# Kernel tuning notes

Measured on AMD Instinct MI355X. Metric: run time of the kernel, lower is better.

The kernel has to match this reference:

```python
import jax, jax.numpy as jnp
import numpy as np

B, T, C, H = 2, 2048, 1024, 16
D = C // H  # head dim = 64
EPS = 1e-5


def layernorm(x, g, b):
    mu = jnp.mean(x, axis=-1, keepdims=True)
    var = jnp.var(x, axis=-1, keepdims=True)
    return (x - mu) * jax.lax.rsqrt(var + EPS) * g + b


def setup_inputs() -> dict:
    key = jax.random.key(0)
    ks = jax.random.split(key, 8)
    init_scale = 0.25
    return {
        "x": jax.random.normal(ks[0], (B, T, C), dtype=jnp.float32),
        # weights stored [in, out] (transpose of torch Linear)
        "w_qkv": jax.random.normal(ks[1], (C, 3 * C), dtype=jnp.float32) * init_scale,
        "b_qkv": jnp.zeros((3 * C,), dtype=jnp.float32),
        "w_proj": jax.random.normal(ks[2], (C, C), dtype=jnp.float32) * init_scale,
        "b_proj": jnp.zeros((C,), dtype=jnp.float32),
        "ln1_g": jnp.ones((C,), dtype=jnp.float32),
        "ln1_b": jnp.zeros((C,), dtype=jnp.float32),
        "w_fc": jax.random.normal(ks[3], (C, 4 * C), dtype=jnp.float32) * init_scale,
        "b_fc": jnp.zeros((4 * C,), dtype=jnp.float32),
        "w_out": jax.random.normal(ks[4], (4 * C, C), dtype=jnp.float32) * init_scale,
        "b_out": jnp.zeros((C,), dtype=jnp.float32),
        "ln2_g": jnp.ones((C,), dtype=jnp.float32),
        "ln2_b": jnp.zeros((C,), dtype=jnp.float32),
    }


def reference(x, w_qkv, b_qkv, w_proj, b_proj, ln1_g, ln1_b,
              w_fc, b_fc, w_out, b_out, ln2_g, ln2_b):
    # ---- attention sub-block (pre-LN) ----
    h = layernorm(x, ln1_g, ln1_b)
    qkv = h @ w_qkv + b_qkv                      # [B,T,3C]
    q, k, v = jnp.split(qkv, 3, axis=-1)
    q = q.reshape(B, T, H, D)
    k = k.reshape(B, T, H, D)
    v = v.reshape(B, T, H, D)
    scores = jnp.einsum('bthd,bshd->bhts', q, k) * (1.0 / np.sqrt(D))
    attn = jax.nn.softmax(scores, axis=-1)       # full [B,H,T,T] as in source
    out = jnp.einsum('bhts,bshd->bthd', attn, v).reshape(B, T, C)
    x = x + out @ w_proj + b_proj
    # ---- MLP sub-block (pre-LN) ----
    h = layernorm(x, ln2_g, ln2_b)
    h = jax.nn.gelu(h @ w_fc + b_fc, approximate=False)  # torch nn.GELU default = exact
    x = x + h @ w_out + b_out
    return x
```

## Files before the change

### kernel.cpp

```cpp
#include <hip/hip_runtime.h>
#include <hip/hip_bf16.h>
#include <math.h>

#define DEVINL static __device__ __forceinline__

typedef _Float16 f16x8 __attribute__((ext_vector_type(8)));
typedef _Float16 f16x4 __attribute__((ext_vector_type(4)));
typedef float f32x4 __attribute__((ext_vector_type(4)));

constexpr int TT = 2048, CC = 1024, HH = 16, DD = 64;

DEVINL void gload_lds16(const void* g, void* s) {
  __builtin_amdgcn_global_load_lds(
      (const __attribute__((address_space(1))) void*)g,
      (__attribute__((address_space(3))) void*)s, 16, 0, 0);
}

__global__ __launch_bounds__(256) void transpose_cast(
    const float* __restrict__ in, _Float16* __restrict__ out, int K, int N) {
  __shared__ float tile[32][33];
  int n0 = blockIdx.x * 32, k0 = blockIdx.y * 32;
  int tx = threadIdx.x & 31, ty = threadIdx.x >> 5;
  #pragma unroll
  for (int i = 0; i < 32; i += 8)
    tile[ty + i][tx] = in[(size_t)(k0 + ty + i) * N + n0 + tx];
  __syncthreads();
  #pragma unroll
  for (int i = 0; i < 32; i += 8)
    out[(size_t)(n0 + ty + i) * K + k0 + tx] = (_Float16)tile[tx][ty + i];
}

__global__ __launch_bounds__(256) void ln_cast(
    const float* __restrict__ x, const float* __restrict__ g,
    const float* __restrict__ bta, _Float16* __restrict__ out) {
  int row = blockIdx.x, t = threadIdx.x;
  float4 v = ((const float4*)(x + (size_t)row * CC))[t];
  float s = v.x + v.y + v.z + v.w;
  float s2 = v.x * v.x + v.y * v.y + v.z * v.z + v.w * v.w;
  #pragma unroll
  for (int o = 32; o >= 1; o >>= 1) { s += __shfl_xor(s, o); s2 += __shfl_xor(s2, o); }
  __shared__ float ss[4], ssq[4];
  int w = t >> 6;
  if ((t & 63) == 0) { ss[w] = s; ssq[w] = s2; }
  __syncthreads();
  s = ss[0] + ss[1] + ss[2] + ss[3];
  s2 = ssq[0] + ssq[1] + ssq[2] + ssq[3];
  float mu = s * (1.0f / CC);
  float rs = rsqrtf(s2 * (1.0f / CC) - mu * mu + 1e-5f);
  float4 gv = ((const float4*)g)[t];
  float4 bv = ((const float4*)bta)[t];
  f16x4 o4;
  o4[0] = (_Float16)((v.x - mu) * rs * gv.x + bv.x);
  o4[1] = (_Float16)((v.y - mu) * rs * gv.y + bv.y);
  o4[2] = (_Float16)((v.z - mu) * rs * gv.z + bv.z);
  o4[3] = (_Float16)((v.w - mu) * rs * gv.w + bv.w);
  ((f16x4*)(out + (size_t)row * CC))[t] = o4;
}

template <int EPI, int N, int K>
__global__ __launch_bounds__(256) void gemm_bt(
    const _Float16* __restrict__ A, const _Float16* __restrict__ Bt,
    const float* __restrict__ bias, const float* __restrict__ res,
    void* __restrict__ outp) {
  __shared__ __align__(16) _Float16 As[128 * 64];
  __shared__ __align__(16) _Float16 Bs[128 * 64];
  const int bm0 = blockIdx.y * 128, bn0 = blockIdx.x * 128;
  const int t = threadIdx.x, w = t >> 6, l = t & 63, lg = l >> 4, lr = l & 15;
  const int wr = w >> 1, wc = w & 1;
  const int srow = t >> 3, sc = t & 7;
  f32x4 acc[4][4] = {};
  for (int k0 = 0; k0 < K; k0 += 64) {
    #pragma unroll
    for (int q = 0; q < 4; ++q) {
      int row = q * 32 + srow;
      int gc = sc ^ (row & 7);
      gload_lds16(A + (size_t)(bm0 + row) * K + k0 + gc * 8, As + row * 64 + sc * 8);
      gload_lds16(Bt + (size_t)(bn0 + row) * K + k0 + gc * 8, Bs + row * 64 + sc * 8);
    }
    __syncthreads();
    #pragma unroll
    for (int ks = 0; ks < 2; ++ks) {
      f16x8 af[4], bfr[4];
      #pragma unroll
      for (int mi = 0; mi < 4; ++mi) {
        int row = wr * 64 + mi * 16 + lr;
        af[mi] = *(const f16x8*)(As + row * 64 + (((ks * 4 + lg) ^ (row & 7)) << 3));
      }
      #pragma unroll
      for (int ni = 0; ni < 4; ++ni) {
        int row = wc * 64 + ni * 16 + lr;
        bfr[ni] = *(const f16x8*)(Bs + row * 64 + (((ks * 4 + lg) ^ (row & 7)) << 3));
      }
      #pragma unroll
      for (int mi = 0; mi < 4; ++mi)
        #pragma unroll
        for (int ni = 0; ni < 4; ++ni)
          acc[mi][ni] = __builtin_amdgcn_mfma_f32_16x16x32_f16(af[mi], bfr[ni], acc[mi][ni], 0, 0, 0);
    }
    __syncthreads();
  }
  #pragma unroll
  for (int mi = 0; mi < 4; ++mi) {
    #pragma unroll
    for (int ni = 0; ni < 4; ++ni) {
      int gc = bn0 + wc * 64 + ni * 16 + lr;
      float bv = bias[gc];
      #pragma unroll
      for (int r = 0; r < 4; ++r) {
        int gr = bm0 + wr * 64 + mi * 16 + lg * 4 + r;
        float v = acc[mi][ni][r] + bv;
        if constexpr (EPI == 1) {
          float gl = 0.5f * v * (1.0f + erff(v * 0.70710678118654752f));
          ((_Float16*)outp)[(size_t)gr * N + gc] = (_Float16)gl;
        } else {
          ((float*)outp)[(size_t)gr * N + gc] = res[(size_t)gr * N + gc] + v;
        }
      }
    }
  }
}

__global__ __launch_bounds__(256) void gemm_qkv(
    const _Float16* __restrict__ A, const _Float16* __restrict__ Bt,
    const float* __restrict__ bias,
    _Float16* __restrict__ qo, _Float16* __restrict__ ko,
    _Float16* __restrict__ vt) {
  __shared__ __align__(16) _Float16 As[128 * 64];
  __shared__ __align__(16) _Float16 Bs[128 * 64];
  const int bm0 = blockIdx.y * 128, bn0 = blockIdx.x * 128;
  const int t = threadIdx.x, w = t >> 6, l = t & 63, lg = l >> 4, lr = l & 15;
  const int wr = w >> 1, wc = w & 1;
  const int srow = t >> 3, sc = t & 7;
  f32x4 acc[4][4] = {};
  for (int k0 = 0; k0 < 1024; k0 += 64) {
    #pragma unroll
    for (int q = 0; q < 4; ++q) {
      int row = q * 32 + srow;
      int gc = sc ^ (row & 7);
      gload_lds16(A + (size_t)(bm0 + row) * 1024 + k0 + gc * 8, As + row * 64 + sc * 8);
      gload_lds16(Bt + (size_t)(bn0 + row) * 1024 + k0 + gc * 8, Bs + row * 64 + sc * 8);
    }
    __syncthreads();
    #pragma unroll
    for (int ks = 0; ks < 2; ++ks) {
      f16x8 af[4], bfr[4];
      #pragma unroll
      for (int mi = 0; mi < 4; ++mi) {
        int row = wr * 64 + mi * 16 + lr;
        af[mi] = *(const f16x8*)(As + row * 64 + (((ks * 4 + lg) ^ (row & 7)) << 3));
      }
      #pragma unroll
      for (int ni = 0; ni < 4; ++ni) {
        int row = wc * 64 + ni * 16 + lr;
        bfr[ni] = *(const f16x8*)(Bs + row * 64 + (((ks * 4 + lg) ^ (row & 7)) << 3));
      }
      #pragma unroll
      for (int mi = 0; mi < 4; ++mi)
        #pragma unroll
        for (int ni = 0; ni < 4; ++ni)
          acc[mi][ni] = __builtin_amdgcn_mfma_f32_16x16x32_f16(af[mi], bfr[ni], acc[mi][ni], 0, 0, 0);
    }
    __syncthreads();
  }
  const float QSCL = 0.125f * 1.44269504f;
  #pragma unroll
  for (int mi = 0; mi < 4; ++mi) {
    #pragma unroll
    for (int ni = 0; ni < 4; ++ni) {
      int gc = bn0 + wc * 64 + ni * 16 + lr;
      float bv = bias[gc];
      int sec = gc >> 10, cc = gc & 1023;
      #pragma unroll
      for (int r = 0; r < 4; ++r) {
        int gr = bm0 + wr * 64 + mi * 16 + lg * 4 + r;
        float v = acc[mi][ni][r] + bv;
        if (sec == 0) {
          qo[(size_t)gr * 1024 + cc] = (_Float16)(v * QSCL);
        } else if (sec == 1) {
          ko[(size_t)gr * 1024 + cc] = (_Float16)v;
        } else {
          int hh = cc >> 6, dd = cc & 63;
          int bb = gr >> 11, tk = gr & (TT - 1);
          vt[(((size_t)bb * HH + hh) * DD + dd) * TT + tk] = (_Float16)v;
        }
      }
    }
  }
}

__global__ __launch_bounds__(256) void flash_attn(
    const _Float16* __restrict__ qg, const _Float16* __restrict__ kg,
    const _Float16* __restrict__ vt, _Float16* __restrict__ att) {
  const int qt0 = blockIdx.x * 64, h = blockIdx.y, b = blockIdx.z;
  const int t = threadIdx.x, w = t >> 6, l = t & 63, lg = l >> 4, lr = l & 15;
  __shared__ __align__(16) _Float16 Ks[2][64 * 64];
  __shared__ __align__(16) _Float16 VTs[2][64 * 64];
  __shared__ __align__(16) _Float16 Ps[4][16 * 64];
  const int srow = t >> 3, sc = t & 7;
  f16x8 qf[2];
  #pragma unroll
  for (int ks = 0; ks < 2; ++ks)
    qf[ks] = *(const f16x8*)(qg + ((size_t)(b * TT + qt0 + w * 16 + lr)) * CC +
                             h * DD + ks * 32 + lg * 8);
  f32x4 o[4] = {};
  f32x4 osum = {};
  float mrow[4];
  #pragma unroll
  for (int r = 0; r < 4; ++r) mrow[r] = -3.0e38f;
  const f16x8 ones = {(_Float16)1, (_Float16)1, (_Float16)1, (_Float16)1,
                      (_Float16)1, (_Float16)1, (_Float16)1, (_Float16)1};

  auto STAGE = [&](int bufi, int kv0) {
    #pragma unroll
    for (int q = 0; q < 2; ++q) {
      int row = q * 32 + srow;
      int gc = sc ^ (row & 7);
      gload_lds16(kg + ((size_t)(b * TT + kv0 + row)) * CC + h * DD + gc * 8,
                  Ks[bufi] + row * 64 + sc * 8);
      gload_lds16(vt + (((size_t)b * HH + h) * DD + row) * TT + kv0 + gc * 8,
                  VTs[bufi] + row * 64 + sc * 8);
    }
  };
  STAGE(0, 0);
  __syncthreads();
  int cur = 0;
  for (int kv0 = 0; kv0 < TT; kv0 += 64) {
    if (kv0 + 64 < TT) STAGE(cur ^ 1, kv0 + 64);
    const _Float16* Kc = Ks[cur];
    const _Float16* Vc = VTs[cur];
    f32x4 s[4] = {};
    #pragma unroll
    for (int ks = 0; ks < 2; ++ks)
      #pragma unroll
      for (int ni = 0; ni < 4; ++ni) {
        int row = ni * 16 + lr;
        f16x8 kf = *(const f16x8*)(Kc + row * 64 + (((ks * 4 + lg) ^ (row & 7)) << 3));
        s[ni] = __builtin_amdgcn_mfma_f32_16x16x32_f16(qf[ks], kf, s[ni], 0, 0, 0);
      }
    float m4[4];
    int ok = 1;
    #pragma unroll
    for (int r = 0; r < 4; ++r) {
      m4[r] = fmaxf(fmaxf(s[0][r], s[1][r]), fmaxf(s[2][r], s[3][r]));
      ok &= (m4[r] <= mrow[r] + 8.0f) ? 1 : 0;
    }
    if (!__all(ok)) {
      #pragma unroll
      for (int r = 0; r < 4; ++r) {
        float rm = m4[r];
        #pragma unroll
        for (int msk = 1; msk <= 8; msk <<= 1) rm = fmaxf(rm, __shfl_xor(rm, msk));
        float mn = fmaxf(mrow[r], rm);
        float corr = exp2f(mrow[r] - mn);
        mrow[r] = mn;
        #pragma unroll
        for (int di = 0; di < 4; ++di) o[di][r] *= corr;
        osum[r] *= corr;
      }
    }
    _Float16* Pw = Ps[w];
    #pragma unroll
    for (int r = 0; r < 4; ++r) {
      float p0 = exp2f(s[0][r] - mrow[r]);
      float p1 = exp2f(s[1][r] - mrow[r]);
      float p2 = exp2f(s[2][r] - mrow[r]);
      float p3 = exp2f(s[3][r] - mrow[r]);
      int prow = lg * 4 + r, rx = prow & 7;
      Pw[prow * 64 + (((0 + (lr >> 3)) ^ rx) << 3) + (lr & 7)] = (_Float16)p0;
      Pw[prow * 64 + (((2 + (lr >> 3)) ^ rx) << 3) + (lr & 7)] = (_Float16)p1;
      Pw[prow * 64 + (((4 + (lr >> 3)) ^ rx) << 3) + (lr & 7)] = (_Float16)p2;
      Pw[prow * 64 + (((6 + (lr >> 3)) ^ rx) << 3) + (lr & 7)] = (_Float16)p3;
    }
    #pragma unroll
    for (int ks = 0; ks < 2; ++ks) {
      f16x8 pf = *(const f16x8*)(Pw + lr * 64 + (((ks * 4 + lg) ^ (lr & 7)) << 3));
      #pragma unroll
      for (int di = 0; di < 4; ++di) {
        int row = di * 16 + lr;
        f16x8 vf = *(const f16x8*)(Vc + row * 64 + (((ks * 4 + lg) ^ (row & 7)) << 3));
        o[di] = __builtin_amdgcn_mfma_f32_16x16x32_f16(pf, vf, o[di], 0, 0, 0);
      }
      osum = __builtin_amdgcn_mfma_f32_16x16x32_f16(pf, ones, osum, 0, 0, 0);
    }
    __syncthreads();
    cur ^= 1;
  }
  #pragma unroll
  for (int r = 0; r < 4; ++r) {
    float rinv = 1.0f / osum[r];
    int row_g = qt0 + w * 16 + lg * 4 + r;
    #pragma unroll
    for (int di = 0; di < 4; ++di)
      att[((size_t)(b * TT + row_g)) * CC + h * DD + di * 16 + lr] =
          (_Float16)(o[di][r] * rinv);
  }
}

extern "C" void kernel_launch(void* const* d_in, const int* in_sizes, int n_in,
                              void* d_out, int out_size, void* d_ws, size_t ws_size,
                              hipStream_t stream) {
  const float* x      = (const float*)d_in[0];
  const float* w_qkv  = (const float*)d_in[1];
  const float* b_qkv  = (const float*)d_in[2];
  const float* w_proj = (const float*)d_in[3];
  const float* b_proj = (const float*)d_in[4];
  const float* ln1_g  = (const float*)d_in[5];
  const float* ln1_b  = (const float*)d_in[6];
  const float* w_fc   = (const float*)d_in[7];
  const float* b_fc   = (const float*)d_in[8];
  const float* w_out  = (const float*)d_in[9];
  const float* b_out  = (const float*)d_in[10];
  const float* ln2_g  = (const float*)d_in[11];
  const float* ln2_b  = (const float*)d_in[12];

  char* ws = (char*)d_ws;
  _Float16* wqkv_t = (_Float16*)(ws);
  _Float16* wproj_t= (_Float16*)(ws + 6291456);
  _Float16* wfc_t  = (_Float16*)(ws + 8388608);
  _Float16* wout_t = (_Float16*)(ws + 16777216);
  _Float16* hslot  = (_Float16*)(ws + 25165824);
  _Float16* qbuf   = (_Float16*)(ws + 33554432);
  _Float16* kbuf   = (_Float16*)(ws + 41943040);
  _Float16* vtbuf  = (_Float16*)(ws + 50331648);
  _Float16* tbuf   = (_Float16*)(ws + 33554432);
  float*    x1     = (float*)(ws + 67108864);

  transpose_cast<<<dim3(96, 32), 256, 0, stream>>>(w_qkv, wqkv_t, 1024, 3072);
  transpose_cast<<<dim3(32, 32), 256, 0, stream>>>(w_proj, wproj_t, 1024, 1024);
  transpose_cast<<<dim3(128, 32), 256, 0, stream>>>(w_fc, wfc_t, 1024, 4096);
  transpose_cast<<<dim3(32, 128), 256, 0, stream>>>(w_out, wout_t, 4096, 1024);

  ln_cast<<<4096, 256, 0, stream>>>(x, ln1_g, ln1_b, hslot);
  gemm_qkv<<<dim3(24, 32), 256, 0, stream>>>(hslot, wqkv_t, b_qkv, qbuf, kbuf, vtbuf);
  flash_attn<<<dim3(32, 16, 2), 256, 0, stream>>>(qbuf, kbuf, vtbuf, hslot);
  gemm_bt<2, 1024, 1024><<<dim3(8, 32), 256, 0, stream>>>(hslot, wproj_t, b_proj, x, x1);
  ln_cast<<<4096, 256, 0, stream>>>(x1, ln2_g, ln2_b, hslot);
  gemm_bt<1, 4096, 1024><<<dim3(32, 32), 256, 0, stream>>>(hslot, wfc_t, b_fc, nullptr, tbuf);
  gemm_bt<2, 1024, 4096><<<dim3(8, 32), 256, 0, stream>>>(tbuf, wout_t, b_out, x1, (float*)d_out);
}
```

Measured before the change: 343.4 us.

## Narrow N-tiles for 1024-wide GEMMs and tune flash attention scheduling

The GEMM kernel gains a BN template parameter. The proj and out GEMMs (N=1024) now use 128x64 tiles, doubling their grid from 256 to 512 blocks so the CUs are better filled. Flash attention precomputes its swizzled LDS offsets and base pointers outside the loop, adds s_setprio around its MFMA sections, and sets a launch-bounds occupancy hint of 4. Narrower tiles lower per-block arithmetic intensity, and the occupancy hint may force register spills.

```diff
diff --git a/kernel.cpp b/kernel.cpp
--- a/kernel.cpp
+++ b/kernel.cpp
@@ -57,33 +57,40 @@
   ((f16x4*)(out + (size_t)row * CC))[t] = o4;
 }
 
-template <int EPI, int N, int K>
+template <int EPI, int N, int K, int BN>
 __global__ __launch_bounds__(256) void gemm_bt(
     const _Float16* __restrict__ A, const _Float16* __restrict__ Bt,
     const float* __restrict__ bias, const float* __restrict__ res,
     void* __restrict__ outp) {
+  constexpr int NWN = BN / 64;
+  constexpr int MI = 2 * NWN;
   __shared__ __align__(16) _Float16 As[128 * 64];
-  __shared__ __align__(16) _Float16 Bs[128 * 64];
-  const int bm0 = blockIdx.y * 128, bn0 = blockIdx.x * 128;
+  __shared__ __align__(16) _Float16 Bs[BN * 64];
+  const int bm0 = blockIdx.y * 128, bn0 = blockIdx.x * BN;
   const int t = threadIdx.x, w = t >> 6, l = t & 63, lg = l >> 4, lr = l & 15;
-  const int wr = w >> 1, wc = w & 1;
+  const int wr = w / NWN, wc = w % NWN;
   const int srow = t >> 3, sc = t & 7;
-  f32x4 acc[4][4] = {};
+  f32x4 acc[MI][4] = {};
   for (int k0 = 0; k0 < K; k0 += 64) {
     #pragma unroll
     for (int q = 0; q < 4; ++q) {
       int row = q * 32 + srow;
       int gc = sc ^ (row & 7);
       gload_lds16(A + (size_t)(bm0 + row) * K + k0 + gc * 8, As + row * 64 + sc * 8);
+    }
+    #pragma unroll
+    for (int q = 0; q < BN / 32; ++q) {
+      int row = q * 32 + srow;
+      int gc = sc ^ (row & 7);
       gload_lds16(Bt + (size_t)(bn0 + row) * K + k0 + gc * 8, Bs + row * 64 + sc * 8);
     }
     __syncthreads();
     #pragma unroll
     for (int ks = 0; ks < 2; ++ks) {
-      f16x8 af[4], bfr[4];
-      #pragma unroll
-      for (int mi = 0; mi < 4; ++mi) {
-        int row = wr * 64 + mi * 16 + lr;
+      f16x8 af[MI], bfr[4];
+      #pragma unroll
+      for (int mi = 0; mi < MI; ++mi) {
+        int row = wr * (16 * MI) + mi * 16 + lr;
         af[mi] = *(const f16x8*)(As + row * 64 + (((ks * 4 + lg) ^ (row & 7)) << 3));
       }
       #pragma unroll
@@ -92,7 +99,7 @@
         bfr[ni] = *(const f16x8*)(Bs + row * 64 + (((ks * 4 + lg) ^ (row & 7)) << 3));
       }
       #pragma unroll
-      for (int mi = 0; mi < 4; ++mi)
+      for (int mi = 0; mi < MI; ++mi)
         #pragma unroll
         for (int ni = 0; ni < 4; ++ni)
           acc[mi][ni] = __builtin_amdgcn_mfma_f32_16x16x32_f16(af[mi], bfr[ni], acc[mi][ni], 0, 0, 0);
@@ -100,14 +107,14 @@
     __syncthreads();
   }
   #pragma unroll
-  for (int mi = 0; mi < 4; ++mi) {
+  for (int mi = 0; mi < MI; ++mi) {
     #pragma unroll
     for (int ni = 0; ni < 4; ++ni) {
       int gc = bn0 + wc * 64 + ni * 16 + lr;
       float bv = bias[gc];
       #pragma unroll
       for (int r = 0; r < 4; ++r) {
-        int gr = bm0 + wr * 64 + mi * 16 + lg * 4 + r;
+        int gr = bm0 + wr * (16 * MI) + mi * 16 + lg * 4 + r;
         float v = acc[mi][ni][r] + bv;
         if constexpr (EPI == 1) {
           float gl = 0.5f * v * (1.0f + erff(v * 0.70710678118654752f));
@@ -188,7 +195,7 @@
   }
 }
 
-__global__ __launch_bounds__(256) void flash_attn(
+__global__ __launch_bounds__(256, 4) void flash_attn(
     const _Float16* __restrict__ qg, const _Float16* __restrict__ kg,
     const _Float16* __restrict__ vt, _Float16* __restrict__ att) {
   const int qt0 = blockIdx.x * 64, h = blockIdx.y, b = blockIdx.z;
@@ -197,6 +204,27 @@
   __shared__ __align__(16) _Float16 VTs[2][64 * 64];
   __shared__ __align__(16) _Float16 Ps[4][16 * 64];
   const int srow = t >> 3, sc = t & 7;
+  const int gcs = sc ^ (srow & 7);
+  const int dk0 = srow * 64 + sc * 8;
+  const _Float16* kg_b = kg + ((size_t)b * TT + srow) * CC + h * DD + gcs * 8;
+  const _Float16* vt_b = vt + (((size_t)b * HH + h) * DD + srow) * TT + gcs * 8;
+  int fro[2][4], pfo[2], pwo[4][4];
+  #pragma unroll
+  for (int ks = 0; ks < 2; ++ks) {
+    #pragma unroll
+    for (int ni = 0; ni < 4; ++ni) {
+      int row = ni * 16 + lr;
+      fro[ks][ni] = row * 64 + (((ks * 4 + lg) ^ (row & 7)) << 3);
+    }
+    pfo[ks] = lr * 64 + (((ks * 4 + lg) ^ (lr & 7)) << 3);
+  }
+  #pragma unroll
+  for (int r = 0; r < 4; ++r) {
+    int prow = lg * 4 + r, rx = prow & 7;
+    #pragma unroll
+    for (int ni = 0; ni < 4; ++ni)
+      pwo[r][ni] = prow * 64 + (((2 * ni + (lr >> 3)) ^ rx) << 3) + (lr & 7);
+  }
   f16x8 qf[2];
   #pragma unroll
   for (int ks = 0; ks < 2; ++ks)
@@ -213,12 +241,8 @@
   auto STAGE = [&](int bufi, int kv0) {
     #pragma unroll
     for (int q = 0; q < 2; ++q) {
-      int row = q * 32 + srow;
-      int gc = sc ^ (row & 7);
-      gload_lds16(kg + ((size_t)(b * TT + kv0 + row)) * CC + h * DD + gc * 8,
-                  Ks[bufi] + row * 64 + sc * 8);
-      gload_lds16(vt + (((size_t)b * HH + h) * DD + row) * TT + kv0 + gc * 8,
-                  VTs[bufi] + row * 64 + sc * 8);
+      gload_lds16(kg_b + (size_t)(kv0 + q * 32) * CC, Ks[bufi] + q * 2048 + dk0);
+      gload_lds16(vt_b + q * 32 * TT + kv0, VTs[bufi] + q * 2048 + dk0);
     }
   };
   STAGE(0, 0);
@@ -229,14 +253,15 @@
     const _Float16* Kc = Ks[cur];
     const _Float16* Vc = VTs[cur];
     f32x4 s[4] = {};
+    __builtin_amdgcn_s_setprio(1);
     #pragma unroll
     for (int ks = 0; ks < 2; ++ks)
       #pragma unroll
       for (int ni = 0; ni < 4; ++ni) {
-        int row = ni * 16 + lr;
-        f16x8 kf = *(const f16x8*)(Kc + row * 64 + (((ks * 4 + lg) ^ (row & 7)) << 3));
+        f16x8 kf = *(const f16x8*)(Kc + fro[ks][ni]);
         s[ni] = __builtin_amdgcn_mfma_f32_16x16x32_f16(qf[ks], kf, s[ni], 0, 0, 0);
       }
+    __builtin_amdgcn_s_setprio(0);
     float m4[4];
     int ok = 1;
     #pragma unroll
@@ -261,27 +286,23 @@
     _Float16* Pw = Ps[w];
     #pragma unroll
     for (int r = 0; r < 4; ++r) {
-      float p0 = exp2f(s[0][r] - mrow[r]);
-      float p1 = exp2f(s[1][r] - mrow[r]);
-      float p2 = exp2f(s[2][r] - mrow[r]);
-      float p3 = exp2f(s[3][r] - mrow[r]);
-      int prow = lg * 4 + r, rx = prow & 7;
-      Pw[prow * 64 + (((0 + (lr >> 3)) ^ rx) << 3) + (lr & 7)] = (_Float16)p0;
-      Pw[prow * 64 + (((2 + (lr >> 3)) ^ rx) << 3) + (lr & 7)] = (_Float16)p1;
-      Pw[prow * 64 + (((4 + (lr >> 3)) ^ rx) << 3) + (lr & 7)] = (_Float16)p2;
-      Pw[prow * 64 + (((6 + (lr >> 3)) ^ rx) << 3) + (lr & 7)] = (_Float16)p3;
-    }
+      Pw[pwo[r][0]] = (_Float16)exp2f(s[0][r] - mrow[r]);
+      Pw[pwo[r][1]] = (_Float16)exp2f(s[1][r] - mrow[r]);
+      Pw[pwo[r][2]] = (_Float16)exp2f(s[2][r] - mrow[r]);
+      Pw[pwo[r][3]] = (_Float16)exp2f(s[3][r] - mrow[r]);
+    }
+    __builtin_amdgcn_s_setprio(1);
     #pragma unroll
     for (int ks = 0; ks < 2; ++ks) {
-      f16x8 pf = *(const f16x8*)(Pw + lr * 64 + (((ks * 4 + lg) ^ (lr & 7)) << 3));
+      f16x8 pf = *(const f16x8*)(Pw + pfo[ks]);
       #pragma unroll
       for (int di = 0; di < 4; ++di) {
-        int row = di * 16 + lr;
-        f16x8 vf = *(const f16x8*)(Vc + row * 64 + (((ks * 4 + lg) ^ (row & 7)) << 3));
+        f16x8 vf = *(const f16x8*)(Vc + fro[ks][di]);
         o[di] = __builtin_amdgcn_mfma_f32_16x16x32_f16(pf, vf, o[di], 0, 0, 0);
       }
       osum = __builtin_amdgcn_mfma_f32_16x16x32_f16(pf, ones, osum, 0, 0, 0);
     }
+    __builtin_amdgcn_s_setprio(0);
     __syncthreads();
     cur ^= 1;
   }
@@ -333,8 +354,8 @@
   ln_cast<<<4096, 256, 0, stream>>>(x, ln1_g, ln1_b, hslot);
   gemm_qkv<<<dim3(24, 32), 256, 0, stream>>>(hslot, wqkv_t, b_qkv, qbuf, kbuf, vtbuf);
   flash_attn<<<dim3(32, 16, 2), 256, 0, stream>>>(qbuf, kbuf, vtbuf, hslot);
-  gemm_bt<2, 1024, 1024><<<dim3(8, 32), 256, 0, stream>>>(hslot, wproj_t, b_proj, x, x1);
+  gemm_bt<2, 1024, 1024, 64><<<dim3(16, 32), 256, 0, stream>>>(hslot, wproj_t, b_proj, x, x1);
   ln_cast<<<4096, 256, 0, stream>>>(x1, ln2_g, ln2_b, hslot);
-  gemm_bt<1, 4096, 1024><<<dim3(32, 32), 256, 0, stream>>>(hslot, wfc_t, b_fc, nullptr, tbuf);
-  gemm_bt<2, 1024, 4096><<<dim3(8, 32), 256, 0, stream>>>(tbuf, wout_t, b_out, x1, (float*)d_out);
-}
+  gemm_bt<1, 4096, 1024, 128><<<dim3(32, 32), 256, 0, stream>>>(hslot, wfc_t, b_fc, nullptr, tbuf);
+  gemm_bt<2, 1024, 4096, 64><<<dim3(16, 32), 256, 0, stream>>>(tbuf, wout_t, b_out, x1, (float*)d_out);
+}
```

Result: faster. 313.2 us (-8.8%).
